# Optimization experiments

Hardware: AMD Instinct MI355X
Metric: run time of the kernel (lower is better)

The kernel has to match this reference:

```python
import jax, jax.numpy as jnp
import numpy as np

N = 50000      # nodes
E = 800000     # edges
F = 64         # in_channels == out_channels
ED = 16        # edge_dim
G = 64         # graphs in batch
L = 2          # numLayers
BN_EPS = 1e-5
STD_EPS = 1e-5
AGG_DIM = F * 4 * 3  # 4 aggregators x 3 scalers


def setup_inputs() -> dict:
    key = jax.random.key(0)
    ks = jax.random.split(key, 12)
    r = lambda k, shp, fan: (jax.random.normal(k, shp, jnp.float32) / np.sqrt(fan)).astype(jnp.float32)
    return dict(
        x=jax.random.normal(ks[0], (N, F), jnp.float32),
        edge_attr=jax.random.normal(ks[1], (E, ED), jnp.float32),
        We=r(ks[2], (L, ED, F), ED), be=jnp.zeros((L, F), jnp.float32),
        Wpre=r(ks[3], (L, 3 * F, F), 3 * F), bpre=jnp.zeros((L, F), jnp.float32),
        Wpost=r(ks[4], (L, F + AGG_DIM, F), F + AGG_DIM), bpost=jnp.zeros((L, F), jnp.float32),
        Wlin=r(ks[5], (L, F, F), F), blin=jnp.zeros((L, F), jnp.float32),
        gamma=jnp.ones((L, F), jnp.float32), beta=jnp.zeros((L, F), jnp.float32),
        W1=r(ks[6], (F, 40), F), b1=jnp.zeros((40,), jnp.float32),
        W2=r(ks[7], (40, 1), 40), b2=jnp.zeros((1,), jnp.float32),
        edge_index=jax.random.randint(ks[8], (2, E), 0, N),
        batch=jnp.sort(jax.random.randint(ks[9], (N,), 0, G)),
    )


def _ceal_conv(x, src, dst, edge_attr, We, be, Wpre, bpre, Wpost, bpost, Wlin, blin, deg, amp, att):
    # PNA-style conv, towers=1, pre_layers=post_layers=1
    e = edge_attr @ We + be                                              # [E,F]
    h = jnp.concatenate([x[dst], x[src], e], axis=-1) @ Wpre + bpre      # [E,F]
    degc = jnp.maximum(deg, 1.0)[:, None]
    mean = jax.ops.segment_sum(h, dst, num_segments=N) / degc
    sq = jax.ops.segment_sum(h * h, dst, num_segments=N) / degc
    std = jnp.sqrt(jax.nn.relu(sq - mean * mean) + STD_EPS)
    has = (deg > 0)[:, None]
    mn = jnp.where(has, jax.ops.segment_min(h, dst, num_segments=N), 0.0)
    mx = jnp.where(has, jax.ops.segment_max(h, dst, num_segments=N), 0.0)
    aggs = jnp.concatenate([mean, mn, mx, std], axis=-1)                 # [N,4F]
    scaled = jnp.concatenate([aggs, aggs * amp[:, None], aggs * att[:, None]], axis=-1)  # [N,12F]
    out = jnp.concatenate([x, scaled], axis=-1) @ Wpost + bpost          # [N,F]
    return out @ Wlin + blin


def _bn(x, gamma, beta):
    mu = x.mean(0)
    var = x.var(0)  # biased, as torch BatchNorm training-mode normalization
    return (x - mu) * jax.lax.rsqrt(var + BN_EPS) * gamma + beta


def reference(x, edge_attr, We, be, Wpre, bpre, Wpost, bpost, Wlin, blin,
              gamma, beta, W1, b1, W2, b2, edge_index, batch):
    src, dst = edge_index[0], edge_index[1]
    deg = jax.ops.segment_sum(jnp.ones((E,), jnp.float32), dst, num_segments=N)
    avg_log = jnp.mean(jnp.log(deg + 1.0))
    logd = jnp.log(jnp.maximum(deg, 1.0) + 1.0)
    amp = logd / avg_log
    att = avg_log / logd
    for l in range(L):
        x = _ceal_conv(x, src, dst, edge_attr, We[l], be[l], Wpre[l], bpre[l],
                       Wpost[l], bpost[l], Wlin[l], blin[l], deg, amp, att)
        x = jax.nn.relu(_bn(x, gamma[l], beta[l]))
    cnt = jnp.maximum(jax.ops.segment_sum(jnp.ones((N,), jnp.float32), batch, num_segments=G), 1.0)
    gm = jax.ops.segment_sum(x, batch, num_segments=G) / cnt[:, None]    # global_mean_pool [G,F]
    return jax.nn.relu(gm @ W1 + b1) @ W2 + b2                           # [G,1]
```

## Files before the change

### kernel.cpp

```cpp
#include <hip/hip_runtime.h>
#include <math.h>
#include <float.h>

#define NN 50000
#define EE 800000
#define FF 64
#define EDIM 16
#define GG 64
#define NB64 782
#define NSB 196

typedef short bf16x8 __attribute__((ext_vector_type(8)));
typedef float f32x4 __attribute__((ext_vector_type(4)));

__device__ inline unsigned short bf_rne(float v) {
  unsigned int u = __float_as_uint(v);
  unsigned int r = (u + 0x7FFFu + ((u >> 16) & 1u)) >> 16;
  return (unsigned short)r;
}
__device__ inline float bf_up(unsigned short h) {
  return __uint_as_float(((unsigned int)h) << 16);
}
__device__ inline void split4(float4 v, ushort4& h, ushort4& l) {
  h.x = bf_rne(v.x); h.y = bf_rne(v.y); h.z = bf_rne(v.z); h.w = bf_rne(v.w);
  l.x = bf_rne(v.x - bf_up(h.x));
  l.y = bf_rne(v.y - bf_up(h.y));
  l.z = bf_rne(v.z - bf_up(h.z));
  l.w = bf_rne(v.w - bf_up(h.w));
}
__device__ inline float blo(unsigned int u) { return __uint_as_float(u << 16); }
__device__ inline float bhi(unsigned int u) { return __uint_as_float(u & 0xFFFF0000u); }

__global__ void k_deg(const int* __restrict__ eidx, int* __restrict__ deg) {
  int e = blockIdx.x * 256 + threadIdx.x;
  if (e < EE) atomicAdd(&deg[eidx[EE + e]], 1);
}

__global__ __launch_bounds__(256) void k_scanA(const int* __restrict__ deg, int* __restrict__ offsets,
                                               int* __restrict__ bsum, float* __restrict__ lsum) {
  __shared__ int ws[4];
  __shared__ float lw[4];
  int t = threadIdx.x;
  int lane = t & 63;
  int wv = t >> 6;
  int i = blockIdx.x * 256 + t;
  int v = (i < NN) ? deg[i] : 0;
  float lg = (i < NN) ? logf((float)v + 1.0f) : 0.0f;
  int x = v;
  #pragma unroll
  for (int o = 1; o < 64; o <<= 1) {
    int y = __shfl_up(x, o);
    if (lane >= o) x += y;
  }
  #pragma unroll
  for (int o = 1; o < 64; o <<= 1) lg += __shfl_xor(lg, o);
  if (lane == 63) ws[wv] = x;
  if (lane == 0) lw[wv] = lg;
  __syncthreads();
  int pre = 0;
  for (int k = 0; k < wv; k++) pre += ws[k];
  if (i < NN) offsets[i] = pre + x - v;
  if (t == 0) {
    bsum[blockIdx.x] = ws[0] + ws[1] + ws[2] + ws[3];
    lsum[blockIdx.x] = lw[0] + lw[1] + lw[2] + lw[3];
  }
}

__global__ __launch_bounds__(256) void k_scanB(const int* __restrict__ bsum, const float* __restrict__ lsum,
                                               int* __restrict__ bpref, float* __restrict__ meta,
                                               float* __restrict__ scbA) {
  __shared__ int ws[4];
  __shared__ float lw[4];
  int t = threadIdx.x;
  int lane = t & 63;
  int wv = t >> 6;
  int v = (t < NSB) ? bsum[t] : 0;
  float lg = (t < NSB) ? lsum[t] : 0.0f;
  int x = v;
  #pragma unroll
  for (int o = 1; o < 64; o <<= 1) {
    int y = __shfl_up(x, o);
    if (lane >= o) x += y;
  }
  #pragma unroll
  for (int o = 1; o < 64; o <<= 1) lg += __shfl_xor(lg, o);
  if (lane == 63) ws[wv] = x;
  if (lane == 0) lw[wv] = lg;
  __syncthreads();
  int pre = 0;
  for (int k = 0; k < wv; k++) pre += ws[k];
  if (t < NSB) bpref[t] = pre + x - v;
  if (t == 0) meta[0] = (lw[0] + lw[1] + lw[2] + lw[3]) / (float)NN;
  if (t < 64) { scbA[t] = 1.0f; scbA[64 + t] = 0.0f; }
  if (t == 0) scbA[128] = -FLT_MAX;
}

__global__ __launch_bounds__(256) void k_scanC(int* __restrict__ offsets, const int* __restrict__ bpref,
                                               const int* __restrict__ deg, const float* __restrict__ meta,
                                               float* __restrict__ amp, float* __restrict__ att) {
  int i = blockIdx.x * 256 + threadIdx.x;
  if (i < NN) {
    offsets[i] += bpref[blockIdx.x];
    float d = (float)deg[i];
    float avg = meta[0];
    float logd = logf(fmaxf(d, 1.0f) + 1.0f);
    amp[i] = logd / avg;
    att[i] = avg / logd;
  }
  if (i == 0) offsets[NN] = EE;
}

__global__ void k_scatter(const int* __restrict__ eidx, const int* __restrict__ offsets,
                          int* __restrict__ cursor, int* __restrict__ srcs,
                          const float* __restrict__ eattr, unsigned int* __restrict__ PermEA) {
  int e = blockIdx.x * 256 + threadIdx.x;
  if (e < EE) {
    int s = eidx[e];
    int d = eidx[EE + e];
    int pos = offsets[d] + atomicAdd(&cursor[d], 1);
    srcs[pos] = s;
    const float4* ep = (const float4*)(eattr + (size_t)e * EDIM);
    float4 q0 = ep[0], q1 = ep[1], q2 = ep[2], q3 = ep[3];
    uint4 pa, pb;
    pa.x = (unsigned)bf_rne(q0.x) | ((unsigned)bf_rne(q0.y) << 16);
    pa.y = (unsigned)bf_rne(q0.z) | ((unsigned)bf_rne(q0.w) << 16);
    pa.z = (unsigned)bf_rne(q1.x) | ((unsigned)bf_rne(q1.y) << 16);
    pa.w = (unsigned)bf_rne(q1.z) | ((unsigned)bf_rne(q1.w) << 16);
    pb.x = (unsigned)bf_rne(q2.x) | ((unsigned)bf_rne(q2.y) << 16);
    pb.y = (unsigned)bf_rne(q2.z) | ((unsigned)bf_rne(q2.w) << 16);
    pb.z = (unsigned)bf_rne(q3.x) | ((unsigned)bf_rne(q3.y) << 16);
    pb.w = (unsigned)bf_rne(q3.z) | ((unsigned)bf_rne(q3.w) << 16);
    ((uint4*)PermEA)[(size_t)pos * 2] = pa;
    ((uint4*)PermEA)[(size_t)pos * 2 + 1] = pb;
  }
}

__global__ __launch_bounds__(256) void k_prep2(const float* __restrict__ We, const float* __restrict__ be,
                                               const float* __restrict__ Wpre, const float* __restrict__ bpre,
                                               const float* __restrict__ Wpost, const float* __restrict__ bpost,
                                               const float* __restrict__ Wlin, const float* __restrict__ blin,
                                               unsigned short* __restrict__ MwT_h, unsigned short* __restrict__ MwT_l,
                                               float* __restrict__ bconst,
                                               unsigned short* __restrict__ WcT_h, unsigned short* __restrict__ WcT_l,
                                               unsigned short* __restrict__ WxT_h, unsigned short* __restrict__ WxT_l,
                                               float* __restrict__ bcomb) {
  int id = blockIdx.x * 256 + threadIdx.x;
  if (id < 53248) {
    int k = id >> 6, f = id & 63;
    float a = 0.0f;
    for (int j = 0; j < FF; j++) a += Wpost[(size_t)k * FF + j] * Wlin[j * FF + f];
    unsigned short h = bf_rne(a);
    WcT_h[f * 832 + k] = h;
    WcT_l[f * 832 + k] = bf_rne(a - bf_up(h));
  } else if (id < 61440) {
    int lid = id - 53248;
    int j = lid >> 6, k = lid & 63;
    float v = (j < 64) ? Wpre[k * FF + j] : Wpre[(64 + k) * FF + (j - 64)];
    unsigned short h = bf_rne(v);
    WxT_h[j * 64 + k] = h;
    WxT_l[j * 64 + k] = bf_rne(v - bf_up(h));
  } else if (id < 62464) {
    int lid = id - 61440;
    int k = lid >> 6, f = lid & 63;
    float a = 0.0f;
    for (int j = 0; j < FF; j++) a += We[k * FF + j] * Wpre[(128 + j) * FF + f];
    unsigned short h = bf_rne(a);
    MwT_h[f * 16 + k] = h;
    MwT_l[f * 16 + k] = bf_rne(a - bf_up(h));
  } else {
    int f = threadIdx.x;
    if (blockIdx.x == 244 && f < 64) {
      float b = bpre[f];
      for (int j = 0; j < FF; j++) b += be[j] * Wpre[(128 + j) * FF + f];
      bconst[f] = b;
      float c = blin[f];
      for (int j = 0; j < FF; j++) c += bpost[j] * Wlin[j * FF + f];
      bcomb[f] = c;
    }
  }
}

__global__ __launch_bounds__(256) void k_xform(const float* __restrict__ x, const float* __restrict__ scb,
                                               const unsigned short* __restrict__ WxT_h,
                                               const unsigned short* __restrict__ WxT_l,
                                               float* __restrict__ Xd, unsigned short* __restrict__ Xs) {
  __shared__ unsigned short Ah[64 * 72], Al[64 * 72];
  __shared__ unsigned short Bh[128 * 72], Bl[128 * 72];
  int t = threadIdx.x;
  int n0 = blockIdx.x * 64;
  {
    int j = t >> 1, half = t & 1;
    const ushort4* srch = (const ushort4*)(WxT_h + j * 64 + half * 32);
    const ushort4* srcl = (const ushort4*)(WxT_l + j * 64 + half * 32);
    #pragma unroll
    for (int i = 0; i < 8; i++) {
      *(ushort4*)&Bh[j * 72 + half * 32 + i * 4] = srch[i];
      *(ushort4*)&Bl[j * 72 + half * 32 + i * 4] = srcl[i];
    }
  }
  {
    int r = t >> 2, c0 = (t & 3) * 16;
    int n = n0 + r;
    bool rok = n < NN;
    const float4* src = (const float4*)(x + (size_t)n * FF + c0);
    float flr = scb[128];
    #pragma unroll
    for (int c4 = 0; c4 < 4; c4++) {
      float4 v = rok ? src[c4] : make_float4(0.f, 0.f, 0.f, 0.f);
      float4 sc = ((const float4*)scb)[(c0 >> 2) + c4];
      float4 of = ((const float4*)(scb + 64))[(c0 >> 2) + c4];
      v.x = fmaxf(v.x * sc.x + of.x, flr);
      v.y = fmaxf(v.y * sc.y + of.y, flr);
      v.z = fmaxf(v.z * sc.z + of.z, flr);
      v.w = fmaxf(v.w * sc.w + of.w, flr);
      ushort4 h4, l4;
      split4(v, h4, l4);
      *(ushort4*)&Ah[r * 72 + c0 + c4 * 4] = h4;
      *(ushort4*)&Al[r * 72 + c0 + c4 * 4] = l4;
    }
  }
  __syncthreads();
  int lane = t & 63;
  int l15 = lane & 15;
  int quad = lane >> 4;
  int w = __builtin_amdgcn_readfirstlane(t >> 6);
  int rbase = (w & 1) * 32;
  int cbase = (w >> 1) * 64;
  f32x4 acc[2][4];
  #pragma unroll
  for (int rt = 0; rt < 2; rt++)
    #pragma unroll
    for (int ct = 0; ct < 4; ct++) acc[rt][ct] = (f32x4){0.f, 0.f, 0.f, 0.f};

  #pragma unroll
  for (int ks = 0; ks < 2; ks++) {
    bf16x8 a_h[2], a_l[2];
    #pragma unroll
    for (int rt = 0; rt < 2; rt++) {
      int row = rbase + rt * 16 + l15;
      a_h[rt] = *(const bf16x8*)&Ah[row * 72 + ks * 32 + quad * 8];
      a_l[rt] = *(const bf16x8*)&Al[row * 72 + ks * 32 + quad * 8];
    }
    #pragma unroll
    for (int ct = 0; ct < 4; ct++) {
      int col = cbase + ct * 16 + l15;
      bf16x8 b_h = *(const bf16x8*)&Bh[col * 72 + ks * 32 + quad * 8];
      bf16x8 b_l = *(const bf16x8*)&Bl[col * 72 + ks * 32 + quad * 8];
      #pragma unroll
      for (int rt = 0; rt < 2; rt++) {
        acc[rt][ct] = __builtin_amdgcn_mfma_f32_16x16x32_bf16(a_h[rt], b_h, acc[rt][ct], 0, 0, 0);
        acc[rt][ct] = __builtin_amdgcn_mfma_f32_16x16x32_bf16(a_h[rt], b_l, acc[rt][ct], 0, 0, 0);
        acc[rt][ct] = __builtin_amdgcn_mfma_f32_16x16x32_bf16(a_l[rt], b_h, acc[rt][ct], 0, 0, 0);
      }
    }
  }
  #pragma unroll
  for (int rt = 0; rt < 2; rt++) {
    #pragma unroll
    for (int ct = 0; ct < 4; ct++) {
      int col = cbase + ct * 16 + l15;
      #pragma unroll
      for (int reg = 0; reg < 4; reg++) {
        int n = n0 + rbase + rt * 16 + quad * 4 + reg;
        if (n < NN) {
          float v = acc[rt][ct][reg];
          if (col < 64) Xd[(size_t)n * FF + col] = v;
          else          Xs[(size_t)n * FF + (col - 64)] = bf_rne(v);
        }
      }
    }
  }
}

__global__ __launch_bounds__(256) void k_agg(const int* __restrict__ srcs, const int* __restrict__ offsets,
                                             const unsigned int* __restrict__ PermEA,
                                             const unsigned short* __restrict__ MwT_h,
                                             const unsigned short* __restrict__ MwT_l,
                                             const float* __restrict__ bconst,
                                             const float* __restrict__ Xd, const unsigned short* __restrict__ Xs,
                                             unsigned short* __restrict__ aggs) {
  __shared__ float et_lds[4][32 * 64];
  int wid = __builtin_amdgcn_readfirstlane(threadIdx.x >> 6);
  int lane = threadIdx.x & 63;
  int l15 = lane & 15;
  int quad = lane >> 4;
  int n = blockIdx.x * 4 + wid;
  if (n >= NN) return;
  float* et_w = et_lds[wid];

  bf16x8 bh[4], bl[4];
  #pragma unroll
  for (int ct = 0; ct < 4; ct++) {
    if (quad < 2) {
      bh[ct] = *(const bf16x8*)&MwT_h[(ct * 16 + l15) * 16 + quad * 8];
      bl[ct] = *(const bf16x8*)&MwT_l[(ct * 16 + l15) * 16 + quad * 8];
    } else {
      bh[ct] = (bf16x8){0, 0, 0, 0, 0, 0, 0, 0};
      bl[ct] = (bf16x8){0, 0, 0, 0, 0, 0, 0, 0};
    }
  }

  float base_h = Xd[(size_t)n * FF + lane] + bconst[lane];
  int o0 = offsets[n], o1 = offsets[n + 1];
  float s = 0.f, sq = 0.f, mn = FLT_MAX, mx = -FLT_MAX;

  for (int base = o0; base < o1; base += 32) {
    int m = min(32, o1 - base);
    int idx = base + (lane & 31);
    int sv = (idx < o1) ? srcs[idx] : 0;

    #pragma unroll
    for (int c = 0; c < 2; c++) {
      if (c * 16 < m) {
        int pos = base + c * 16 + l15;
        pos = min(pos, EE - 1);
        bf16x8 af = (bf16x8){0, 0, 0, 0, 0, 0, 0, 0};
        if (quad < 2) af = *(const bf16x8*)(PermEA + (size_t)pos * 8 + quad * 4);
        #pragma unroll
        for (int ct = 0; ct < 4; ct++) {
          f32x4 acc = (f32x4){0.f, 0.f, 0.f, 0.f};
          acc = __builtin_amdgcn_mfma_f32_16x16x32_bf16(af, bl[ct], acc, 0, 0, 0);
          acc = __builtin_amdgcn_mfma_f32_16x16x32_bf16(af, bh[ct], acc, 0, 0, 0);
          int row = c * 16 + quad * 4;
          #pragma unroll
          for (int reg = 0; reg < 4; reg++)
            et_w[(row + reg) * 64 + ct * 16 + l15] = acc[reg];
        }
      }
    }

    for (int j = 0; j < m; j++) {
      int src = __shfl(sv, j);
      float xs = bf_up(Xs[(size_t)src * FF + lane]);
      float h = base_h + xs + et_w[j * 64 + lane];
      s += h;
      sq += h * h;
      mn = fminf(mn, h);
      mx = fmaxf(mx, h);
    }
  }
  float d = (float)(o1 - o0);
  float dc = fmaxf(d, 1.0f);
  float mean = s / dc;
  float msq = sq / dc;
  float sd = sqrtf(fmaxf(msq - mean * mean, 0.0f) + 1e-5f);
  bool has = d > 0.0f;
  float vmn = has ? mn : 0.0f;
  float vmx = has ? mx : 0.0f;
  size_t b = (size_t)n * 256;
  aggs[b + lane] = bf_rne(mean);
  aggs[b + 64 + lane] = bf_rne(vmn);
  aggs[b + 128 + lane] = bf_rne(vmx);
  aggs[b + 192 + lane] = bf_rne(sd);
}

__global__ __launch_bounds__(256) void k_post(const float* __restrict__ x, const float* __restrict__ scb,
                                              const unsigned short* __restrict__ aggs,
                                              const float* __restrict__ amp, const float* __restrict__ att,
                                              const unsigned short* __restrict__ WcT_h,
                                              const unsigned short* __restrict__ WcT_l,
                                              const float* __restrict__ bcomb,
                                              float* __restrict__ y, float* __restrict__ partials) {
  __shared__ unsigned short Ah[64 * 72], Al[64 * 72];
  __shared__ unsigned short Bh[64 * 72], Bl[64 * 72];
  __shared__ float red_s[4][32], red_q[4][32];
  int t = threadIdx.x;
  int n0 = blockIdx.x * 64;
  int lane = t & 63;
  int l15 = lane & 15;
  int quad = lane >> 4;
  int w = __builtin_amdgcn_readfirstlane(t >> 6);
  int rbase = (w & 1) * 32;
  int cbase = (w >> 1) * 32;

  int ar = t >> 2;
  int ac0 = (t & 3) * 16;
  int an = n0 + ar;
  bool rok = an < NN;
  float sc_amp = rok ? amp[an] : 0.f;
  float sc_att = rok ? att[an] : 0.f;
  const float* xrow = x + (size_t)an * FF;
  const unsigned short* arow = aggs + (size_t)an * 256;
  float flr = scb[128];

  f32x4 acc[2][2];
  #pragma unroll
  for (int rt = 0; rt < 2; rt++)
    #pragma unroll
    for (int ct = 0; ct < 2; ct++) acc[rt][ct] = (f32x4){0.f, 0.f, 0.f, 0.f};

  for (int kc = 0; kc < 13; kc++) {
    if (kc == 0) {
      #pragma unroll
      for (int c4 = 0; c4 < 4; c4++) {
        float4 v = rok ? *(const float4*)(xrow + ac0 + c4 * 4) : make_float4(0.f, 0.f, 0.f, 0.f);
        float4 sc = ((const float4*)scb)[(ac0 >> 2) + c4];
        float4 of = ((const float4*)(scb + 64))[(ac0 >> 2) + c4];
        v.x = fmaxf(v.x * sc.x + of.x, flr);
        v.y = fmaxf(v.y * sc.y + of.y, flr);
        v.z = fmaxf(v.z * sc.z + of.z, flr);
        v.w = fmaxf(v.w * sc.w + of.w, flr);
        ushort4 h4, l4;
        split4(v, h4, l4);
        *(ushort4*)&Ah[ar * 72 + ac0 + c4 * 4] = h4;
        *(ushort4*)&Al[ar * 72 + ac0 + c4 * 4] = l4;
      }
    } else {
      int kcm = kc - 1;
      const unsigned short* srcb = arow + (kcm & 3) * 64;
      int sel = kcm >> 2;
      float scale = (sel == 0) ? 1.0f : (sel == 1 ? sc_amp : sc_att);
      #pragma unroll
      for (int c4 = 0; c4 < 4; c4++) {
        ushort4 u = rok ? *(const ushort4*)(srcb + ac0 + c4 * 4) : make_ushort4(0, 0, 0, 0);
        ushort4 h4;
        h4.x = bf_rne(bf_up(u.x) * scale);
        h4.y = bf_rne(bf_up(u.y) * scale);
        h4.z = bf_rne(bf_up(u.z) * scale);
        h4.w = bf_rne(bf_up(u.w) * scale);
        *(ushort4*)&Ah[ar * 72 + ac0 + c4 * 4] = h4;
      }
    }
    {
      int kbase = kc * 64;
      const ushort4* sh = (const ushort4*)(WcT_h + ar * 832 + kbase + ac0);
      const ushort4* sl = (const ushort4*)(WcT_l + ar * 832 + kbase + ac0);
      #pragma unroll
      for (int i = 0; i < 4; i++) {
        *(ushort4*)&Bh[ar * 72 + ac0 + i * 4] = sh[i];
        *(ushort4*)&Bl[ar * 72 + ac0 + i * 4] = sl[i];
      }
    }
    __syncthreads();
    bool full = (kc == 0);
    #pragma unroll
    for (int ks = 0; ks < 2; ks++) {
      bf16x8 a_h[2], a_l[2], b_h[2], b_l[2];
      #pragma unroll
      for (int rt = 0; rt < 2; rt++) {
        int row = rbase + rt * 16 + l15;
        a_h[rt] = *(const bf16x8*)&Ah[row * 72 + ks * 32 + quad * 8];
        if (full) a_l[rt] = *(const bf16x8*)&Al[row * 72 + ks * 32 + quad * 8];
      }
      #pragma unroll
      for (int ct = 0; ct < 2; ct++) {
        int col = cbase + ct * 16 + l15;
        b_h[ct] = *(const bf16x8*)&Bh[col * 72 + ks * 32 + quad * 8];
        b_l[ct] = *(const bf16x8*)&Bl[col * 72 + ks * 32 + quad * 8];
      }
      #pragma unroll
      for (int rt = 0; rt < 2; rt++)
        #pragma unroll
        for (int ct = 0; ct < 2; ct++) {
          acc[rt][ct] = __builtin_amdgcn_mfma_f32_16x16x32_bf16(a_h[rt], b_h[ct], acc[rt][ct], 0, 0, 0);
          acc[rt][ct] = __builtin_amdgcn_mfma_f32_16x16x32_bf16(a_h[rt], b_l[ct], acc[rt][ct], 0, 0, 0);
          if (full)
            acc[rt][ct] = __builtin_amdgcn_mfma_f32_16x16x32_bf16(a_l[rt], b_h[ct], acc[rt][ct], 0, 0, 0);
        }
    }
    __syncthreads();
  }

  float ps[2] = {0.f, 0.f}, pq[2] = {0.f, 0.f};
  #pragma unroll
  for (int ct = 0; ct < 2; ct++) {
    int col = cbase + ct * 16 + l15;
    float bc = bcomb[col];
    #pragma unroll
    for (int rt = 0; rt < 2; rt++) {
      #pragma unroll
      for (int reg = 0; reg < 4; reg++) {
        int n = n0 + rbase + rt * 16 + quad * 4 + reg;
        float v = acc[rt][ct][reg] + bc;
        if (n < NN) {
          y[(size_t)n * FF + col] = v;
          ps[ct] += v;
          pq[ct] += v * v;
        }
      }
    }
  }
  #pragma unroll
  for (int ct = 0; ct < 2; ct++) {
    ps[ct] += __shfl_xor(ps[ct], 16);
    ps[ct] += __shfl_xor(ps[ct], 32);
    pq[ct] += __shfl_xor(pq[ct], 16);
    pq[ct] += __shfl_xor(pq[ct], 32);
  }
  if (quad == 0) {
    #pragma unroll
    for (int ct = 0; ct < 2; ct++) {
      red_s[w][ct * 16 + l15] = ps[ct];
      red_q[w][ct * 16 + l15] = pq[ct];
    }
  }
  __syncthreads();
  if (t < 64) {
    float ss, qq;
    if (t < 32) { ss = red_s[0][t] + red_s[1][t]; qq = red_q[0][t] + red_q[1][t]; }
    else        { ss = red_s[2][t - 32] + red_s[3][t - 32]; qq = red_q[2][t - 32] + red_q[3][t - 32]; }
    partials[(size_t)blockIdx.x * 128 + t] = ss;
    partials[(size_t)blockIdx.x * 128 + 64 + t] = qq;
  }
}

__global__ __launch_bounds__(1024) void k_bnfin(const float* __restrict__ partials,
                                                const float* __restrict__ gamma, const float* __restrict__ beta,
                                                float* __restrict__ scb) {
  __shared__ float red[1024];
  __shared__ double tot[128];
  int t = threadIdx.x;
  int c = t & 127, seg = t >> 7;
  float s = 0.f;
  for (int i = seg; i < NB64; i += 8) s += partials[(size_t)i * 128 + c];
  red[t] = s;
  __syncthreads();
  if (t < 128) {
    double d = 0.0;
    #pragma unroll
    for (int sg = 0; sg < 8; sg++) d += (double)red[sg * 128 + t];
    tot[t] = d;
  }
  __syncthreads();
  if (t < 64) {
    double mu = tot[t] / (double)NN;
    double var = tot[64 + t] / (double)NN - mu * mu;
    float sc = gamma[t] * rsqrtf((float)fmax(var, 0.0) + 1e-5f);
    scb[t] = sc;
    scb[64 + t] = beta[t] - (float)mu * sc;
  }
  if (t == 0) scb[128] = 0.0f;
}

__global__ __launch_bounds__(256) void k_pool(const float* __restrict__ x, const float* __restrict__ scb,
                                              const int* __restrict__ batch,
                                              float* __restrict__ psum, float* __restrict__ cnt) {
  int lane = threadIdx.x & 63;
  int wv = threadIdx.x >> 6;
  int wglobal = blockIdx.x * 4 + wv;
  int nw = gridDim.x * 4;
  int per = (NN + nw - 1) / nw;
  int n0 = wglobal * per;
  int n1 = min(n0 + per, NN);
  if (n0 >= n1) return;
  float sc = scb[lane], of = scb[64 + lane], flr = scb[128];
  int gcur = batch[n0];
  float acc = 0.0f;
  int count = 0;
  for (int n = n0; n < n1; n++) {
    int g = batch[n];
    float v = fmaxf(x[(size_t)n * FF + lane] * sc + of, flr);
    if (g != gcur) {
      atomicAdd(&psum[gcur * FF + lane], acc);
      if (lane == 0) atomicAdd(&cnt[gcur], (float)count);
      gcur = g; acc = 0.0f; count = 0;
    }
    acc += v;
    count++;
  }
  atomicAdd(&psum[gcur * FF + lane], acc);
  if (lane == 0) atomicAdd(&cnt[gcur], (float)count);
}

__global__ void k_final(const float* __restrict__ psum, const float* __restrict__ cnt,
                        const float* __restrict__ W1, const float* __restrict__ b1,
                        const float* __restrict__ W2, const float* __restrict__ b2, float* __restrict__ out) {
  int g = threadIdx.x;
  if (g >= GG) return;
  float c = fmaxf(cnt[g], 1.0f);
  float gm[64];
  #pragma unroll
  for (int i = 0; i < 64; i++) gm[i] = psum[g * FF + i] / c;
  float o = b2[0];
  for (int h = 0; h < 40; h++) {
    float a = b1[h];
    #pragma unroll
    for (int i = 0; i < 64; i++) a += gm[i] * W1[i * 40 + h];
    o += fmaxf(a, 0.0f) * W2[h];
  }
  out[g] = o;
}

extern "C" void kernel_launch(void* const* d_in, const int* in_sizes, int n_in,
                              void* d_out, int out_size, void* d_ws, size_t ws_size,
                              hipStream_t stream) {
  (void)in_sizes; (void)n_in; (void)out_size; (void)ws_size;
  const float* x0    = (const float*)d_in[0];
  const float* eattr = (const float*)d_in[1];
  const float* We    = (const float*)d_in[2];
  const float* be    = (const float*)d_in[3];
  const float* Wpre  = (const float*)d_in[4];
  const float* bpre  = (const float*)d_in[5];
  const float* Wpost = (const float*)d_in[6];
  const float* bpost = (const float*)d_in[7];
  const float* Wlin  = (const float*)d_in[8];
  const float* blin  = (const float*)d_in[9];
  const float* gamma = (const float*)d_in[10];
  const float* beta  = (const float*)d_in[11];
  const float* W1    = (const float*)d_in[12];
  const float* b1    = (const float*)d_in[13];
  const float* W2    = (const float*)d_in[14];
  const float* b2    = (const float*)d_in[15];
  const int* eidx    = (const int*)d_in[16];
  const int* batch   = (const int*)d_in[17];
  float* out = (float*)d_out;

  char* w = (char*)d_ws;
  size_t off = 0;
  auto alloc = [&](size_t bytes) -> void* {
    void* p = w + off;
    off += bytes;
    off = (off + 255) & ~(size_t)255;
    return p;
  };
  int*    deg     = (int*)alloc(NN * sizeof(int));
  int*    offsets = (int*)alloc((NN + 1) * sizeof(int));
  int*    cursor  = (int*)alloc(NN * sizeof(int));
  int*    srcs    = (int*)alloc(EE * sizeof(int));
  unsigned int* PermEA = (unsigned int*)alloc(((size_t)EE + 16) * 8 * sizeof(unsigned int));
  int*    bsum    = (int*)alloc(NSB * sizeof(int));
  int*    bpref   = (int*)alloc(NSB * sizeof(int));
  float*  lsum    = (float*)alloc(NSB * sizeof(float));
  float*  meta    = (float*)alloc(sizeof(float));
  float*  amp     = (float*)alloc(NN * sizeof(float));
  float*  att     = (float*)alloc(NN * sizeof(float));
  unsigned short* MwT_h = (unsigned short*)alloc(FF * EDIM * sizeof(unsigned short));
  unsigned short* MwT_l = (unsigned short*)alloc(FF * EDIM * sizeof(unsigned short));
  float*  bconst  = (float*)alloc(FF * sizeof(float));
  float*  bcomb   = (float*)alloc(FF * sizeof(float));
  float*  scbA    = (float*)alloc(129 * sizeof(float));
  float*  scbB    = (float*)alloc(2 * 129 * sizeof(float));
  unsigned short* WcT_h = (unsigned short*)alloc(FF * 832 * sizeof(unsigned short));
  unsigned short* WcT_l = (unsigned short*)alloc(FF * 832 * sizeof(unsigned short));
  unsigned short* WxT_h = (unsigned short*)alloc(128 * 64 * sizeof(unsigned short));
  unsigned short* WxT_l = (unsigned short*)alloc(128 * 64 * sizeof(unsigned short));
  float*  partials = (float*)alloc((size_t)NB64 * 128 * sizeof(float));
  float*  Xd      = (float*)alloc((size_t)NN * FF * sizeof(float));
  unsigned short* Xs = (unsigned short*)alloc((size_t)NN * FF * sizeof(unsigned short));
  unsigned short* aggs = (unsigned short*)alloc((size_t)NN * 256 * sizeof(unsigned short));
  float*  ybuf    = (float*)alloc((size_t)NN * FF * sizeof(float));
  float*  psum    = (float*)alloc((GG * FF + GG) * sizeof(float));
  float*  cnt     = psum + GG * FF;

  hipMemsetAsync(deg, 0, NN * sizeof(int), stream);
  hipMemsetAsync(cursor, 0, NN * sizeof(int), stream);
  hipMemsetAsync(psum, 0, (GG * FF + GG) * sizeof(float), stream);

  k_deg<<<(EE + 255) / 256, 256, 0, stream>>>(eidx, deg);
  k_scanA<<<NSB, 256, 0, stream>>>(deg, offsets, bsum, lsum);
  k_scanB<<<1, 256, 0, stream>>>(bsum, lsum, bpref, meta, scbA);
  k_scanC<<<NSB, 256, 0, stream>>>(offsets, bpref, deg, meta, amp, att);
  k_scatter<<<(EE + 255) / 256, 256, 0, stream>>>(eidx, offsets, cursor, srcs, eattr, PermEA);

  const float* xin = x0;
  const float* scb_in = scbA;
  for (int l = 0; l < 2; l++) {
    k_prep2<<<245, 256, 0, stream>>>(We + l * EDIM * FF, be + l * FF, Wpre + (size_t)l * 3 * FF * FF,
                                     bpre + l * FF, Wpost + (size_t)l * 832 * FF, bpost + l * FF,
                                     Wlin + l * FF * FF, blin + l * FF,
                                     MwT_h, MwT_l, bconst, WcT_h, WcT_l, WxT_h, WxT_l, bcomb);
    k_xform<<<NB64, 256, 0, stream>>>(xin, scb_in, WxT_h, WxT_l, Xd, Xs);
    k_agg<<<(NN + 3) / 4, 256, 0, stream>>>(srcs, offsets, PermEA, MwT_h, MwT_l, bconst, Xd, Xs, aggs);
    k_post<<<NB64, 256, 0, stream>>>(xin, scb_in, aggs, amp, att, WcT_h, WcT_l, bcomb, ybuf, partials);
    k_bnfin<<<1, 1024, 0, stream>>>(partials, gamma + l * FF, beta + l * FF, scbB + l * 129);
    xin = ybuf;
    scb_in = scbB + l * 129;
  }
  k_pool<<<200, 256, 0, stream>>>(ybuf, scbB + 129, batch, psum, cnt);
  k_final<<<1, 64, 0, stream>>>(psum, cnt, W1, b1, W2, b2, out);
}
```

Baseline: 654.3 us.

## Consume edge MFMA results in registers instead of staging through LDS

The edge-attribute weight matrix is stored with columns permuted so that each lane's MFMA accumulator holds four contiguous feature columns. The aggregation kernel then combines per-edge terms straight from registers and gathers four source features per lane with vector loads. Per-feature statistics are reduced across quads with shuffles, and the output is written as one vector store per lane. This removes the LDS round trip, the serial per-edge loop and the lane broadcast, at the cost of more registers, masking for partial 16-edge tiles and a clamped gather on out-of-range edges.

Measured after the change: 552.3 us. 15.6% less time.

```diff
diff --git a/kernel.cpp b/kernel.cpp
--- a/kernel.cpp
+++ b/kernel.cpp
@@ -165,8 +165,9 @@
     float a = 0.0f;
     for (int j = 0; j < FF; j++) a += We[k * FF + j] * Wpre[(128 + j) * FF + f];
     unsigned short h = bf_rne(a);
-    MwT_h[f * 16 + k] = h;
-    MwT_l[f * 16 + k] = bf_rne(a - bf_up(h));
+    int ct = f & 3, jcol = f >> 2;
+    MwT_h[(ct * 16 + jcol) * 16 + k] = h;
+    MwT_l[(ct * 16 + jcol) * 16 + k] = bf_rne(a - bf_up(h));
   } else {
     int f = threadIdx.x;
     if (blockIdx.x == 244 && f < 64) {
@@ -279,14 +280,12 @@
                                              const float* __restrict__ bconst,
                                              const float* __restrict__ Xd, const unsigned short* __restrict__ Xs,
                                              unsigned short* __restrict__ aggs) {
-  __shared__ float et_lds[4][32 * 64];
   int wid = __builtin_amdgcn_readfirstlane(threadIdx.x >> 6);
   int lane = threadIdx.x & 63;
   int l15 = lane & 15;
   int quad = lane >> 4;
   int n = blockIdx.x * 4 + wid;
   if (n >= NN) return;
-  float* et_w = et_lds[wid];
 
   bf16x8 bh[4], bl[4];
   #pragma unroll
@@ -300,58 +299,75 @@
     }
   }
 
-  float base_h = Xd[(size_t)n * FF + lane] + bconst[lane];
+  float4 xd4 = *(const float4*)(Xd + (size_t)n * FF + 4 * l15);
+  float4 bc4 = *(const float4*)(bconst + 4 * l15);
+  float bas[4] = {xd4.x + bc4.x, xd4.y + bc4.y, xd4.z + bc4.z, xd4.w + bc4.w};
+
   int o0 = offsets[n], o1 = offsets[n + 1];
-  float s = 0.f, sq = 0.f, mn = FLT_MAX, mx = -FLT_MAX;
-
-  for (int base = o0; base < o1; base += 32) {
-    int m = min(32, o1 - base);
-    int idx = base + (lane & 31);
-    int sv = (idx < o1) ? srcs[idx] : 0;
-
-    #pragma unroll
-    for (int c = 0; c < 2; c++) {
-      if (c * 16 < m) {
-        int pos = base + c * 16 + l15;
-        pos = min(pos, EE - 1);
-        bf16x8 af = (bf16x8){0, 0, 0, 0, 0, 0, 0, 0};
-        if (quad < 2) af = *(const bf16x8*)(PermEA + (size_t)pos * 8 + quad * 4);
-        #pragma unroll
-        for (int ct = 0; ct < 4; ct++) {
-          f32x4 acc = (f32x4){0.f, 0.f, 0.f, 0.f};
-          acc = __builtin_amdgcn_mfma_f32_16x16x32_bf16(af, bl[ct], acc, 0, 0, 0);
-          acc = __builtin_amdgcn_mfma_f32_16x16x32_bf16(af, bh[ct], acc, 0, 0, 0);
-          int row = c * 16 + quad * 4;
-          #pragma unroll
-          for (int reg = 0; reg < 4; reg++)
-            et_w[(row + reg) * 64 + ct * 16 + l15] = acc[reg];
-        }
-      }
-    }
-
-    for (int j = 0; j < m; j++) {
-      int src = __shfl(sv, j);
-      float xs = bf_up(Xs[(size_t)src * FF + lane]);
-      float h = base_h + xs + et_w[j * 64 + lane];
-      s += h;
-      sq += h * h;
-      mn = fminf(mn, h);
-      mx = fmaxf(mx, h);
-    }
-  }
+  float s[4]  = {0.f, 0.f, 0.f, 0.f};
+  float sq[4] = {0.f, 0.f, 0.f, 0.f};
+  float mn[4] = {FLT_MAX, FLT_MAX, FLT_MAX, FLT_MAX};
+  float mx[4] = {-FLT_MAX, -FLT_MAX, -FLT_MAX, -FLT_MAX};
+
+  for (int base = o0; base < o1; base += 16) {
+    bf16x8 af = (bf16x8){0, 0, 0, 0, 0, 0, 0, 0};
+    if (quad < 2) af = *(const bf16x8*)(PermEA + (size_t)(base + l15) * 8 + quad * 4);
+    f32x4 acc[4];
+    #pragma unroll
+    for (int ct = 0; ct < 4; ct++) {
+      f32x4 a = (f32x4){0.f, 0.f, 0.f, 0.f};
+      a = __builtin_amdgcn_mfma_f32_16x16x32_bf16(af, bl[ct], a, 0, 0, 0);
+      a = __builtin_amdgcn_mfma_f32_16x16x32_bf16(af, bh[ct], a, 0, 0, 0);
+      acc[ct] = a;
+    }
+    #pragma unroll
+    for (int reg = 0; reg < 4; reg++) {
+      int e = base + quad * 4 + reg;
+      bool valid = e < o1;
+      int ec = min(e, o1 - 1);
+      int src = srcs[ec];
+      ushort4 xs4 = *(const ushort4*)(Xs + (size_t)src * FF + 4 * l15);
+      float xf[4] = {bf_up(xs4.x), bf_up(xs4.y), bf_up(xs4.z), bf_up(xs4.w)};
+      #pragma unroll
+      for (int ct = 0; ct < 4; ct++) {
+        float h = bas[ct] + xf[ct] + acc[ct][reg];
+        float hv = valid ? h : 0.0f;
+        s[ct] += hv;
+        sq[ct] = fmaf(hv, hv, sq[ct]);
+        float t1 = fminf(mn[ct], h);
+        float t2 = fmaxf(mx[ct], h);
+        mn[ct] = valid ? t1 : mn[ct];
+        mx[ct] = valid ? t2 : mx[ct];
+      }
+    }
+  }
+
+  #pragma unroll
+  for (int ct = 0; ct < 4; ct++) {
+    s[ct] += __shfl_xor(s[ct], 16);  s[ct] += __shfl_xor(s[ct], 32);
+    sq[ct] += __shfl_xor(sq[ct], 16); sq[ct] += __shfl_xor(sq[ct], 32);
+    mn[ct] = fminf(mn[ct], __shfl_xor(mn[ct], 16)); mn[ct] = fminf(mn[ct], __shfl_xor(mn[ct], 32));
+    mx[ct] = fmaxf(mx[ct], __shfl_xor(mx[ct], 16)); mx[ct] = fmaxf(mx[ct], __shfl_xor(mx[ct], 32));
+  }
+
   float d = (float)(o1 - o0);
   float dc = fmaxf(d, 1.0f);
-  float mean = s / dc;
-  float msq = sq / dc;
-  float sd = sqrtf(fmaxf(msq - mean * mean, 0.0f) + 1e-5f);
+  float rdc = 1.0f / dc;
   bool has = d > 0.0f;
-  float vmn = has ? mn : 0.0f;
-  float vmx = has ? mx : 0.0f;
-  size_t b = (size_t)n * 256;
-  aggs[b + lane] = bf_rne(mean);
-  aggs[b + 64 + lane] = bf_rne(vmn);
-  aggs[b + 128 + lane] = bf_rne(vmx);
-  aggs[b + 192 + lane] = bf_rne(sd);
+  ushort4 outv;
+  unsigned short ov[4];
+  #pragma unroll
+  for (int ct = 0; ct < 4; ct++) {
+    float mean = s[ct] * rdc;
+    float msq = sq[ct] * rdc;
+    float sd = sqrtf(fmaxf(msq - mean * mean, 0.0f) + 1e-5f);
+    float vmn = has ? mn[ct] : 0.0f;
+    float vmx = has ? mx[ct] : 0.0f;
+    float val = (quad == 0) ? mean : (quad == 1) ? vmn : (quad == 2) ? vmx : sd;
+    ov[ct] = bf_rne(val);
+  }
+  outv.x = ov[0]; outv.y = ov[1]; outv.z = ov[2]; outv.w = ov[3];
+  *(ushort4*)(aggs + (size_t)n * 256 + quad * 64 + 4 * l15) = outv;
 }
 
 __global__ __launch_bounds__(256) void k_post(const float* __restrict__ x, const float* __restrict__ scb,
```
